# Performance work log

Hardware: AMD Instinct MI355X
Metric: run time of the kernel (lower is better)

## Reference

```python
import jax, jax.numpy as jnp
import numpy as np

DIM = 512
EXP = 2
INNER = EXP * DIM            # 1024
QKV_BLOCK = 64
NH = INNER // QKV_BLOCK      # 16 heads
DH = QKV_BLOCK               # 64 head dim
B, S = 2, 2048
KSZ = 4                      # causal conv kernel size
EPS = 5e-5                   # backend eps
NORM_EPS = 1e-6
CAP = 15.0                   # gate soft cap


def setup_inputs() -> dict:
    key = jax.random.key(0)
    ks = jax.random.split(key, 10)
    sc = lambda d: (2.0 / (5.0 * d)) ** 0.5  # small_init std
    b_if = jnp.concatenate([jnp.zeros(NH), jnp.linspace(3.0, 6.0, NH)]).astype(jnp.float32)
    return {
        "x": jax.random.normal(ks[0], (B, S, DIM), jnp.float32),
        "W_up": (jax.random.normal(ks[1], (2 * INNER, DIM), jnp.float32) * sc(DIM)),
        "W_q": (jax.random.normal(ks[2], (NH, DH, DH), jnp.float32) * sc(DH)),
        "W_k": (jax.random.normal(ks[3], (NH, DH, DH), jnp.float32) * sc(DH)),
        "W_v": (jax.random.normal(ks[4], (NH, DH, DH), jnp.float32) * sc(DH)),
        "conv_w": (jax.random.normal(ks[5], (INNER, KSZ), jnp.float32) * (1.0 / KSZ ** 0.5)),
        "conv_b": jnp.zeros((INNER,), jnp.float32),
        "W_if": (jax.random.normal(ks[6], (2 * NH, 3 * INNER), jnp.float32) * 0.02),
        "b_if": b_if,
        "norm_w": jnp.zeros((INNER,), jnp.float32),  # residual weight: gain = 1 + w
        "skip": jnp.ones((INNER,), jnp.float32),
        "W_down": (jax.random.normal(ks[7], (DIM, INNER), jnp.float32) * (2.0 / 15.0 / INNER ** 0.5)),
    }


def _headwise(x, W):
    # x: (B,S,INNER) -> per-head block-diagonal projection with W: (NH,DH,DH)
    xh = x.reshape(*x.shape[:-1], NH, DH)
    yh = jnp.einsum('bsnd,nod->bsno', xh, W)
    return yh.reshape(*x.shape[:-1], INNER)


def _causal_conv1d(x, w, b):
    # depthwise causal conv along S; x: (B,S,C), w: (C,K), b: (C,)
    xp = jnp.pad(x, ((0, 0), (KSZ - 1, 0), (0, 0)))
    y = b
    for j in range(KSZ):  # fixed tiny kernel loop
        y = y + xp[:, j:j + S, :] * w[:, j]
    return y


def _mlstm_parallel(q, k, v, i, f):
    # q,k,v: (B,NH,S,DH); i,f: (B,NH,S). Stabilized parallel mLSTM (native chunkwise math).
    logf = jax.nn.log_sigmoid(f)
    Fc = jnp.cumsum(logf, axis=-1)                              # (B,NH,S)
    logD = Fc[:, :, :, None] - Fc[:, :, None, :] + i[:, :, None, :]
    mask = jnp.tril(jnp.ones((S, S), bool))
    logD = jnp.where(mask, logD, -jnp.inf)
    m = jnp.max(logD, axis=-1)                                  # (B,NH,S), finite (diag = i[t])
    D = jnp.exp(logD - m[..., None])
    Smat = jnp.einsum('bnsd,bntd->bnst', q, k) * (DH ** -0.5)
    C = Smat * D
    n = jnp.maximum(jnp.abs(C.sum(axis=-1)), jnp.exp(-m))       # normalizer
    return jnp.einsum('bnst,bntd->bnsd', C, v) / (n + EPS)[..., None]


def reference(x, W_up, W_q, W_k, W_v, conv_w, conv_b, W_if, b_if, norm_w, skip, W_down):
    # up-projection and gate split
    x_inner = jnp.einsum('bsd,ed->bse', x, W_up)                # (B,S,2*INNER)
    x_mlstm, z = x_inner[..., :INNER], x_inner[..., INNER:]

    # causal depthwise conv + SiLU
    x_conv_act = jax.nn.silu(_causal_conv1d(x_mlstm, conv_w, conv_b))

    # headwise q,k,v
    q = _headwise(x_conv_act, W_q)
    k = _headwise(x_conv_act, W_k)
    v = _headwise(x_mlstm, W_v)

    # gate preactivations with soft cap
    if_pre = jnp.einsum('bse,ge->bsg', jnp.concatenate([q, k, v], axis=-1), W_if) + b_if
    if_pre = CAP * jnp.tanh(if_pre / CAP)
    i_pre, f_pre = if_pre[..., :NH], if_pre[..., NH:]           # (B,S,NH)
    i_g = i_pre.transpose(0, 2, 1)                              # (B,NH,S)
    f_g = f_pre.transpose(0, 2, 1)

    qh = q.reshape(B, S, NH, DH).transpose(0, 2, 1, 3)
    kh = k.reshape(B, S, NH, DH).transpose(0, 2, 1, 3)
    vh = v.reshape(B, S, NH, DH).transpose(0, 2, 1, 3)

    h = _mlstm_parallel(qh, kh, vh, i_g, f_g)                   # (B,NH,S,DH)

    # multi-head RMSNorm with residual gain (1 + w)
    rrms = jax.lax.rsqrt(jnp.mean(h * h, axis=-1, keepdims=True) + NORM_EPS)
    gain = (1.0 + norm_w).reshape(1, NH, 1, DH)
    h_norm = (h * rrms * gain).transpose(0, 2, 1, 3).reshape(B, S, INNER)

    # learnable skip, output gate, down-projection
    h_tilde = h_norm + skip * x_conv_act
    h_out = h_tilde * jax.nn.silu(z)
    return jnp.einsum('bse,de->bsd', h_out, W_down)
```

## Files before the change

### kernel.cpp

```cpp
#include <hip/hip_runtime.h>
#include <math.h>

constexpr int DIM_   = 512;
constexpr int INNER_ = 1024;
constexpr int NHEAD  = 16;
constexpr int BATCH  = 2;
constexpr int SEQ_   = 2048;
constexpr int TOK    = BATCH * SEQ_;
constexpr float EPS_ = 5e-5f;
constexpr float NEPS = 1e-6f;
constexpr float CAPV = 15.0f;

typedef __bf16 bf16_t;
typedef __attribute__((ext_vector_type(8)))  __bf16 bf16x8;
typedef __attribute__((ext_vector_type(4)))  __bf16 bf16x4;
typedef __attribute__((ext_vector_type(16))) float  f32x16;

template<int BM, int BN, int WM, int WN, int MODE>
__global__ __launch_bounds__(256) void gemm_split(const float* __restrict__ A,
    const float* __restrict__ B, float* __restrict__ C,
    int K, int lda, int ldb, int ldc)
{
    constexpr bool HAS_AL = (MODE >= 2), HAS_BL = (MODE >= 3);
    constexpr int TM = WM / 32, TN = WN / 32, NWC = BN / WN;
    __shared__ __align__(16) bf16_t sAh[BM * 32];
    __shared__ __align__(16) bf16_t sBh[BN * 32];
    __shared__ __align__(16) bf16_t sAl[HAS_AL ? BM * 32 : 8];
    __shared__ __align__(16) bf16_t sBl[HAS_BL ? BN * 32 : 8];
    const int bm = blockIdx.y * BM, bn = blockIdx.x * BN;
    const int tid = threadIdx.x, w = tid >> 6, l = tid & 63;
    const int l31 = l & 31, lh = l >> 5;
    const int wr = w / NWC, wc = w % NWC;
    f32x16 acc[TM][TN];
#pragma unroll
    for (int i = 0; i < TM; ++i)
#pragma unroll
        for (int j = 0; j < TN; ++j)
#pragma unroll
            for (int r = 0; r < 16; ++r) acc[i][j][r] = 0.f;

    for (int k0 = 0; k0 < K; k0 += 32) {
#pragma unroll
        for (int it = 0; it < BM * 4 / 256; ++it) {
            int gi = tid + it * 256; int row = gi >> 2, g = gi & 3;
            const float* src = A + (size_t)(bm + row) * lda + k0 + g * 8;
            float4 u0 = *(const float4*)src, u1 = *(const float4*)(src + 4);
            float va[8] = {u0.x, u0.y, u0.z, u0.w, u1.x, u1.y, u1.z, u1.w};
            bf16x8 h, lo2;
#pragma unroll
            for (int e = 0; e < 8; ++e) {
                bf16_t hv = (bf16_t)va[e]; h[e] = hv;
                if constexpr (HAS_AL) lo2[e] = (bf16_t)(va[e] - (float)hv);
            }
            int off = row * 32 + ((g ^ (row & 3)) << 3);
            *(bf16x8*)&sAh[off] = h;
            if constexpr (HAS_AL) *(bf16x8*)&sAl[off] = lo2;
        }
#pragma unroll
        for (int it = 0; it < BN * 4 / 256; ++it) {
            int gi = tid + it * 256; int row = gi >> 2, g = gi & 3;
            const float* src = B + (size_t)(bn + row) * ldb + k0 + g * 8;
            float4 u0 = *(const float4*)src, u1 = *(const float4*)(src + 4);
            float va[8] = {u0.x, u0.y, u0.z, u0.w, u1.x, u1.y, u1.z, u1.w};
            bf16x8 h, lo2;
#pragma unroll
            for (int e = 0; e < 8; ++e) {
                bf16_t hv = (bf16_t)va[e]; h[e] = hv;
                if constexpr (HAS_BL) lo2[e] = (bf16_t)(va[e] - (float)hv);
            }
            int off = row * 32 + ((g ^ (row & 3)) << 3);
            *(bf16x8*)&sBh[off] = h;
            if constexpr (HAS_BL) *(bf16x8*)&sBl[off] = lo2;
        }
        __syncthreads();
#pragma unroll
        for (int ks = 0; ks < 2; ++ks) {
            const int gk = 2 * ks + lh;
            bf16x8 af[TM], alf[TM], bfv[TN], blf[TN];
#pragma unroll
            for (int i = 0; i < TM; ++i) {
                int row = wr * WM + i * 32 + l31;
                int off = row * 32 + ((gk ^ (row & 3)) << 3);
                af[i] = *(const bf16x8*)&sAh[off];
                if constexpr (HAS_AL) alf[i] = *(const bf16x8*)&sAl[off];
            }
#pragma unroll
            for (int j = 0; j < TN; ++j) {
                int row = wc * WN + j * 32 + l31;
                int off = row * 32 + ((gk ^ (row & 3)) << 3);
                bfv[j] = *(const bf16x8*)&sBh[off];
                if constexpr (HAS_BL) blf[j] = *(const bf16x8*)&sBl[off];
            }
#pragma unroll
            for (int i = 0; i < TM; ++i)
#pragma unroll
                for (int j = 0; j < TN; ++j) {
                    acc[i][j] = __builtin_amdgcn_mfma_f32_32x32x16_bf16(af[i], bfv[j], acc[i][j], 0, 0, 0);
                    if constexpr (HAS_AL)
                        acc[i][j] = __builtin_amdgcn_mfma_f32_32x32x16_bf16(alf[i], bfv[j], acc[i][j], 0, 0, 0);
                    if constexpr (HAS_BL)
                        acc[i][j] = __builtin_amdgcn_mfma_f32_32x32x16_bf16(af[i], blf[j], acc[i][j], 0, 0, 0);
                }
        }
        __syncthreads();
    }
#pragma unroll
    for (int i = 0; i < TM; ++i)
#pragma unroll
        for (int j = 0; j < TN; ++j)
#pragma unroll
            for (int r = 0; r < 16; ++r) {
                int row = bm + wr * WM + i * 32 + (r & 3) + 8 * (r >> 2) + 4 * lh;
                int col = bn + wc * WN + j * 32 + l31;
                C[(size_t)row * ldc + col] = acc[i][j][r];
            }
}

__global__ __launch_bounds__(256) void conv_silu_k(const float* __restrict__ xin,
    const float* __restrict__ cw, const float* __restrict__ cb, float* __restrict__ xca)
{
    const int c = blockIdx.x * 256 + threadIdx.x;
    const int t = blockIdx.y;
    const int s = t & (SEQ_ - 1);
    const float w0 = cw[c*4+0], w1 = cw[c*4+1], w2 = cw[c*4+2], w3 = cw[c*4+3];
    const float* base = xin + (size_t)t * 2048 + c;
    float acc = cb[c];
    if (s >= 3) acc += base[-3*2048] * w0;
    if (s >= 2) acc += base[-2*2048] * w1;
    if (s >= 1) acc += base[-1*2048] * w2;
    acc += base[0] * w3;
    float sg = 1.f / (1.f + __expf(-acc));
    xca[(size_t)t * INNER_ + c] = acc * sg;
}

__global__ __launch_bounds__(256) void wif_cvt(const float* __restrict__ W_if,
    bf16_t* __restrict__ wif16)
{
    int i4 = blockIdx.x * 256 + threadIdx.x;
    float4 v = *(const float4*)(W_if + (size_t)i4 * 4);
    bf16x4 o; o[0]=(bf16_t)v.x; o[1]=(bf16_t)v.y; o[2]=(bf16_t)v.z; o[3]=(bf16_t)v.w;
    *(bf16x4*)(wif16 + (size_t)i4 * 4) = o;
}

__global__ __launch_bounds__(256) void qkv_mfma(const float* __restrict__ xca,
    const float* __restrict__ xin, const float* __restrict__ Wq,
    const float* __restrict__ Wk, const float* __restrict__ Wv,
    bf16_t* __restrict__ qb16, bf16_t* __restrict__ kb16,
    bf16_t* __restrict__ vb16, bf16_t* __restrict__ vbt16)
{
    __shared__ __align__(16) bf16_t Xs[128 * 64];
    __shared__ __align__(16) bf16_t Ws[64 * 64];
    const int mt = blockIdx.x, n = blockIdx.y, which = blockIdx.z;
    const int t0 = mt * 128, b = t0 >> 11, s0 = t0 & (SEQ_ - 1);
    const float* X = (which == 2) ? xin : xca;
    const size_t xpitch = (which == 2) ? 2048 : 1024;
    const float* W = ((which == 0) ? Wq : (which == 1) ? Wk : Wv) + n * 4096;
    const int tid = threadIdx.x, w = tid >> 6, l = tid & 63, l31 = l & 31, lh = l >> 5;
    const size_t gbn = (size_t)(b * NHEAD + n) * SEQ_;

#pragma unroll
    for (int it = 0; it < 4; ++it) {
        int gi = tid + it * 256; int row = gi >> 3, g = gi & 7;
        const float* src = X + (size_t)(t0 + row) * xpitch + n * 64 + g * 8;
        float4 u0 = *(const float4*)src, u1 = *(const float4*)(src + 4);
        float va[8] = {u0.x, u0.y, u0.z, u0.w, u1.x, u1.y, u1.z, u1.w};
        bf16x8 h;
#pragma unroll
        for (int e = 0; e < 8; ++e) h[e] = (bf16_t)va[e];
        *(bf16x8*)&Xs[row * 64 + ((g ^ (row & 7)) << 3)] = h;
    }
#pragma unroll
    for (int it = 0; it < 2; ++it) {
        int gi = tid + it * 256; int row = gi >> 3, g = gi & 7;
        const float* src = W + row * 64 + g * 8;
        float4 u0 = *(const float4*)src, u1 = *(const float4*)(src + 4);
        float va[8] = {u0.x, u0.y, u0.z, u0.w, u1.x, u1.y, u1.z, u1.w};
        bf16x8 h;
#pragma unroll
        for (int e = 0; e < 8; ++e) h[e] = (bf16_t)va[e];
        *(bf16x8*)&Ws[row * 64 + ((g ^ (row & 7)) << 3)] = h;
    }
    __syncthreads();

    if (which < 2) {
        const int wr = w >> 1, wc = w & 1;
        f32x16 acc[2];
#pragma unroll
        for (int i = 0; i < 2; ++i)
#pragma unroll
            for (int r = 0; r < 16; ++r) acc[i][r] = 0.f;
#pragma unroll
        for (int ks = 0; ks < 4; ++ks) {
            const int gk = 2 * ks + lh;
            const int wrow = wc * 32 + l31;
            bf16x8 bfrag = *(const bf16x8*)&Ws[wrow * 64 + ((gk ^ (wrow & 7)) << 3)];
#pragma unroll
            for (int i = 0; i < 2; ++i) {
                int row = wr * 64 + i * 32 + l31;
                bf16x8 afrag = *(const bf16x8*)&Xs[row * 64 + ((gk ^ (row & 7)) << 3)];
                acc[i] = __builtin_amdgcn_mfma_f32_32x32x16_bf16(afrag, bfrag, acc[i], 0, 0, 0);
            }
        }
        bf16_t* dst = which ? kb16 : qb16;
#pragma unroll
        for (int i = 0; i < 2; ++i)
#pragma unroll
            for (int r = 0; r < 16; ++r) {
                int srow = wr * 64 + i * 32 + (r & 3) + 8 * (r >> 2) + 4 * lh;
                dst[(gbn + s0 + srow) * 64 + wc * 32 + l31] = (bf16_t)acc[i][r];
            }
    } else {
        const int dh = w >> 1, th = w & 1;
        f32x16 acc[2];
#pragma unroll
        for (int j = 0; j < 2; ++j)
#pragma unroll
            for (int r = 0; r < 16; ++r) acc[j][r] = 0.f;
#pragma unroll
        for (int ks = 0; ks < 4; ++ks) {
            const int gk = 2 * ks + lh;
            const int wrow = dh * 32 + l31;
            bf16x8 afrag = *(const bf16x8*)&Ws[wrow * 64 + ((gk ^ (wrow & 7)) << 3)];
#pragma unroll
            for (int j = 0; j < 2; ++j) {
                int xrow = th * 64 + j * 32 + l31;
                bf16x8 bfrag = *(const bf16x8*)&Xs[xrow * 64 + ((gk ^ (xrow & 7)) << 3)];
                acc[j] = __builtin_amdgcn_mfma_f32_32x32x16_bf16(afrag, bfrag, acc[j], 0, 0, 0);
            }
        }
        const size_t vtb = (size_t)(b * NHEAD + n) * 64;
#pragma unroll
        for (int j = 0; j < 2; ++j)
#pragma unroll
            for (int r = 0; r < 16; ++r) {
                int drow = dh * 32 + (r & 3) + 8 * (r >> 2) + 4 * lh;
                int tcol = th * 64 + j * 32 + l31;
                vbt16[(vtb + drow) * SEQ_ + s0 + tcol] = (bf16_t)acc[j][r];
            }
        __syncthreads();
#pragma unroll
        for (int j = 0; j < 2; ++j)
#pragma unroll
            for (int r = 0; r < 16; ++r) {
                int tokrow = th * 64 + j * 32 + l31;
                int d = dh * 32 + (r & 3) + 8 * (r >> 2) + 4 * lh;
                Xs[tokrow * 64 + ((((d >> 3) ^ (tokrow & 7))) << 3) + (d & 7)] = (bf16_t)acc[j][r];
            }
        __syncthreads();
#pragma unroll
        for (int it = 0; it < 4; ++it) {
            int gi = tid + it * 256; int row = gi >> 3, g = gi & 7;
            bf16x8 v = *(const bf16x8*)&Xs[row * 64 + ((g ^ (row & 7)) << 3)];
            *(bf16x8*)&vb16[(gbn + s0 + row) * 64 + g * 8] = v;
        }
    }
}

__global__ __launch_bounds__(256) void if_mfma(const bf16_t* __restrict__ qb16,
    const bf16_t* __restrict__ kb16, const bf16_t* __restrict__ vb16,
    const bf16_t* __restrict__ wif16, float* __restrict__ ifp)
{
    __shared__ float red[4][32][33];
    const int t0g = blockIdx.x * 32;
    const int b = t0g >> 11, s0 = t0g & (SEQ_ - 1);
    const int tid = threadIdx.x, w = tid >> 6, l = tid & 63, l31 = l & 31, lh = l >> 5;
    const size_t base0 = (size_t)b * NHEAD * SEQ_ * 64 + (size_t)(s0 + l31) * 64;
    const bf16_t* wbase = wif16 + (size_t)l31 * 3072 + 8 * lh;
    f32x16 acc;
#pragma unroll
    for (int r = 0; r < 16; ++r) acc[r] = 0.f;
#pragma unroll 4
    for (int it = 0; it < 48; ++it) {
        const int kg = w * 768 + it * 16;
        const int which = kg >> 10, rem = kg & 1023;
        const int head = rem >> 6, dd = (rem & 63) + 8 * lh;
        const bf16_t* src = (which == 0) ? qb16 : (which == 1) ? kb16 : vb16;
        bf16x8 af = *(const bf16x8*)(src + base0 + (size_t)head * SEQ_ * 64 + dd);
        bf16x8 bf = *(const bf16x8*)(wbase + kg);
        acc = __builtin_amdgcn_mfma_f32_32x32x16_bf16(af, bf, acc, 0, 0, 0);
    }
#pragma unroll
    for (int r = 0; r < 16; ++r) {
        int row = (r & 3) + 8 * (r >> 2) + 4 * lh;
        red[w][row][l31] = acc[r];
    }
    __syncthreads();
#pragma unroll
    for (int it = 0; it < 4; ++it) {
        int idx = tid + it * 256;
        int row = idx >> 5, col = idx & 31;
        float s = red[0][row][col] + red[1][row][col] + red[2][row][col] + red[3][row][col];
        ifp[(size_t)(t0g + row) * 32 + col] = s;
    }
}

__global__ __launch_bounds__(256) void gate_scan(const float* __restrict__ ifp,
    const float* __restrict__ b_if, float* __restrict__ aval,
    float* __restrict__ cmaxv, float* __restrict__ emv)
{
    __shared__ float tots[256];
    const int bn = blockIdx.x;
    const int b = bn >> 4, n = bn & 15;
    const int tid = threadIdx.x;
    const float bi = b_if[n], bf = b_if[16 + n];
    const int s0 = tid * 8;
    float iv[8], lf[8];
#pragma unroll
    for (int j = 0; j < 8; ++j) {
        size_t row = ((size_t)b * SEQ_ + s0 + j) * 32;
        float ip = ifp[row + n] + bi;        ip = CAPV * tanhf(ip * (1.f / CAPV));
        float fp = ifp[row + 16 + n] + bf;   fp = CAPV * tanhf(fp * (1.f / CAPV));
        float ls = fminf(fp, 0.f) - log1pf(expf(-fabsf(fp)));
        iv[j] = ip; lf[j] = ls;
    }
#pragma unroll
    for (int j = 1; j < 8; ++j) lf[j] += lf[j-1];
    tots[tid] = lf[7];
    __syncthreads();
    for (int off = 1; off < 256; off <<= 1) {
        float o = (tid >= off) ? tots[tid - off] : 0.f;
        __syncthreads();
        tots[tid] += o;
        __syncthreads();
    }
    const float exs = (tid > 0) ? tots[tid - 1] : 0.f;
    float Fc[8], a[8], am[8];
#pragma unroll
    for (int j = 0; j < 8; ++j) { Fc[j] = exs + lf[j]; a[j] = iv[j] - Fc[j]; }
    am[0] = a[0];
#pragma unroll
    for (int j = 1; j < 8; ++j) am[j] = fmaxf(am[j-1], a[j]);
    __syncthreads();
    tots[tid] = am[7];
    __syncthreads();
    for (int off = 1; off < 256; off <<= 1) {
        float o = (tid >= off) ? tots[tid - off] : -INFINITY;
        __syncthreads();
        tots[tid] = fmaxf(tots[tid], o);
        __syncthreads();
    }
    const float exm = (tid > 0) ? tots[tid - 1] : -INFINITY;
    const size_t base = (size_t)bn * SEQ_ + s0;
#pragma unroll
    for (int j = 0; j < 8; ++j) {
        float cm = fmaxf(exm, am[j]);
        aval[base + j]  = a[j];
        cmaxv[base + j] = cm;
        emv[base + j]   = expf(-(Fc[j] + cm));
    }
}

__global__ __launch_bounds__(256, 3) void mlstm_k2(
    const bf16_t* __restrict__ qb16, const bf16_t* __restrict__ kb16,
    const bf16_t* __restrict__ vbt16,
    const float* __restrict__ aval, const float* __restrict__ cmaxv,
    const float* __restrict__ emv, const float* __restrict__ xca,
    const float* __restrict__ xin, const float* __restrict__ norm_w,
    const float* __restrict__ skipv, float* __restrict__ houtp)
{
    __shared__ bf16_t ks[64*64];
    __shared__ bf16_t vts[64*64];
    __shared__ bf16_t Ps[64*64];
    __shared__ float a_sh[64], cm_sh[64], em_sh[64], nw_sh[64], sk_sh[64];
    __shared__ float red_lds[2][2][2][16];

    const int st = (int)gridDim.x - 1 - (int)blockIdx.x;
    const int n = blockIdx.y, b = blockIdx.z;
    const int tid = threadIdx.x;
    const int w = tid >> 6, l = tid & 63;
    const int rh = w >> 1, th = w & 1;
    const int l31 = l & 31, lh = l >> 5;
    const size_t gb = (size_t)(b * NHEAD + n) * SEQ_;

    if (tid < 64) {
        cm_sh[tid] = cmaxv[gb + st*64 + tid];
        em_sh[tid] = emv[gb + st*64 + tid];
        nw_sh[tid] = 1.f + norm_w[n*64 + tid];
        sk_sh[tid] = skipv[n*64 + tid];
    }
    bf16x8 qf[4];
    {
        const bf16_t* qp = qb16 + (gb + (size_t)st*64 + 32*rh + l31) * 64 + 8*lh;
#pragma unroll
        for (int kc = 0; kc < 4; ++kc) qf[kc] = *(const bf16x8*)(qp + 16*kc);
    }
    f32x16 hac, csum;
#pragma unroll
    for (int i = 0; i < 16; ++i) { hac[i] = 0.f; csum[i] = 0.f; }
    __syncthreads();

    for (int tt = 0; tt <= st; ++tt) {
        {
            const bf16_t* kgp = kb16 + (gb + (size_t)tt*64) * 64;
            const bf16_t* vgp = vbt16 + (size_t)(b * NHEAD + n) * 64 * SEQ_ + (size_t)tt*64;
#pragma unroll
            for (int it = 0; it < 2; ++it) {
                int id = tid + it * 256;
                int r = id >> 3, c = (id & 7) << 3;
                int sw = c ^ ((r & 7) << 3);
                bf16x8 kv = *(const bf16x8*)(kgp + r*64 + c);
                *(bf16x8*)(&ks[r*64 + sw]) = kv;
                bf16x8 vv = *(const bf16x8*)(vgp + (size_t)r * SEQ_ + c);
                *(bf16x8*)(&vts[r*64 + sw]) = vv;
            }
            if (tid < 64) a_sh[tid] = aval[gb + tt*64 + tid];
        }
        __syncthreads();
        f32x16 acc;
#pragma unroll
        for (int i = 0; i < 16; ++i) acc[i] = 0.f;
        {
            const int r = l31 + 32*th;
            const int swb = (r & 7) << 3;
#pragma unroll
            for (int kc = 0; kc < 4; ++kc) {
                bf16x8 bk = *(const bf16x8*)(&ks[r*64 + ((8*lh + 16*kc) ^ swb)]);
                acc = __builtin_amdgcn_mfma_f32_32x32x16_bf16(qf[kc], bk, acc, 0, 0, 0);
            }
        }
        {
            const int tcol = l31 + 32*th;
            const float aw = a_sh[tcol];
            const bool diag = (tt == st);
#pragma unroll
            for (int reg = 0; reg < 16; ++reg) {
                const int srow = (reg & 3) + 8*(reg >> 2) + 4*lh + 32*rh;
                float wgt = 0.125f * __expf(aw - cm_sh[srow]);
                if (diag && tcol > srow) wgt = 0.f;
                float p = acc[reg] * wgt;
                csum[reg] += p;
                Ps[srow*64 + (tcol ^ ((srow & 7) << 3))] = (bf16_t)p;
            }
        }
        __syncthreads();
        {
            const int pr = l31 + 32*rh, vr = l31 + 32*th;
            const int swp = (pr & 7) << 3, swv = (vr & 7) << 3;
#pragma unroll
            for (int kc = 0; kc < 4; ++kc) {
                const int d0 = 8*lh + 16*kc;
                bf16x8 ap = *(const bf16x8*)(&Ps[pr*64 + (d0 ^ swp)]);
                bf16x8 bv = *(const bf16x8*)(&vts[vr*64 + (d0 ^ swv)]);
                hac = __builtin_amdgcn_mfma_f32_32x32x16_bf16(ap, bv, hac, 0, 0, 0);
            }
        }
        __syncthreads();
    }

#pragma unroll
    for (int reg = 0; reg < 16; ++reg) {
        float c = csum[reg];
        c += __shfl_xor(c, 1); c += __shfl_xor(c, 2); c += __shfl_xor(c, 4);
        c += __shfl_xor(c, 8); c += __shfl_xor(c, 16);
        csum[reg] = c;
    }
    if (l31 == 0) {
#pragma unroll
        for (int reg = 0; reg < 16; ++reg) red_lds[rh][th][lh][reg] = csum[reg];
    }
    __syncthreads();
    float sqv[16];
#pragma unroll
    for (int reg = 0; reg < 16; ++reg) {
        const int srow = (reg & 3) + 8*(reg >> 2) + 4*lh + 32*rh;
        float ct = red_lds[rh][0][lh][reg] + red_lds[rh][1][lh][reg];
        float iv = 1.f / (fmaxf(fabsf(ct), em_sh[srow]) + EPS_);
        hac[reg] *= iv;
        sqv[reg] = hac[reg] * hac[reg];
    }
    __syncthreads();
#pragma unroll
    for (int reg = 0; reg < 16; ++reg) {
        float sq = sqv[reg];
        sq += __shfl_xor(sq, 1); sq += __shfl_xor(sq, 2); sq += __shfl_xor(sq, 4);
        sq += __shfl_xor(sq, 8); sq += __shfl_xor(sq, 16);
        sqv[reg] = sq;
    }
    if (l31 == 0) {
#pragma unroll
        for (int reg = 0; reg < 16; ++reg) red_lds[rh][th][lh][reg] = sqv[reg];
    }
    __syncthreads();
    {
        const int dcol = l31 + 32*th;
        const float gn = nw_sh[dcol], sk = sk_sh[dcol];
        const int col = n*64 + dcol;
#pragma unroll
        for (int reg = 0; reg < 16; ++reg) {
            const int srow = (reg & 3) + 8*(reg >> 2) + 4*lh + 32*rh;
            float sq = red_lds[rh][0][lh][reg] + red_lds[rh][1][lh][reg];
            float rr = rsqrtf(sq * (1.f/64.f) + NEPS);
            const size_t tok = (size_t)b * SEQ_ + (size_t)st*64 + srow;
            float ht = hac[reg] * rr * gn + sk * xca[tok * INNER_ + col];
            float zz = xin[tok * 2048 + 1024 + col];
            float sil = zz / (1.f + __expf(-zz));
            houtp[tok * 2048 + col] = ht * sil;
        }
    }
}

extern "C" void kernel_launch(void* const* d_in, const int* in_sizes, int n_in,
                              void* d_out, int out_size, void* d_ws, size_t ws_size,
                              hipStream_t stream)
{
    const float* x      = (const float*)d_in[0];
    const float* W_up   = (const float*)d_in[1];
    const float* W_q    = (const float*)d_in[2];
    const float* W_k    = (const float*)d_in[3];
    const float* W_v    = (const float*)d_in[4];
    const float* conv_w = (const float*)d_in[5];
    const float* conv_b = (const float*)d_in[6];
    const float* W_if   = (const float*)d_in[7];
    const float* b_if   = (const float*)d_in[8];
    const float* norm_w = (const float*)d_in[9];
    const float* skip   = (const float*)d_in[10];
    const float* W_down = (const float*)d_in[11];
    float* out = (float*)d_out;

    float* xin   = (float*)d_ws;
    float* xca   = xin  + (size_t)TOK * 2048;
    float* ifp   = xca  + (size_t)TOK * INNER_;
    float* aval  = ifp  + (size_t)TOK * 32;
    float* cmaxv = aval + (size_t)BATCH * NHEAD * SEQ_;
    float* emv   = cmaxv+ (size_t)BATCH * NHEAD * SEQ_;
    bf16_t* qb16 = (bf16_t*)(emv + (size_t)BATCH * NHEAD * SEQ_);
    bf16_t* kb16 = qb16 + (size_t)TOK * INNER_;
    bf16_t* vb16 = kb16 + (size_t)TOK * INNER_;
    bf16_t* vbt16= vb16 + (size_t)TOK * INNER_;
    bf16_t* wif16= vbt16+ (size_t)TOK * INNER_;

    gemm_split<128,128,64,64,3><<<dim3(2048/128, TOK/128), 256, 0, stream>>>(
        x, W_up, xin, DIM_, DIM_, DIM_, 2048);
    conv_silu_k<<<dim3(INNER_/256, TOK), 256, 0, stream>>>(xin, conv_w, conv_b, xca);
    wif_cvt<<<dim3(96), 256, 0, stream>>>(W_if, wif16);
    qkv_mfma<<<dim3(TOK/128, NHEAD, 3), 256, 0, stream>>>(xca, xin, W_q, W_k, W_v,
        qb16, kb16, vb16, vbt16);
    if_mfma<<<dim3(TOK/32), 256, 0, stream>>>(qb16, kb16, vb16, wif16, ifp);
    gate_scan<<<dim3(BATCH*NHEAD), 256, 0, stream>>>(ifp, b_if, aval, cmaxv, emv);
    mlstm_k2<<<dim3(SEQ_/64, NHEAD, BATCH), 256, 0, stream>>>(qb16, kb16, vbt16,
        aval, cmaxv, emv, xca, xin, norm_w, skip, xin );
    gemm_split<128,64,32,64,3><<<dim3(DIM_/64, TOK/128), 256, 0, stream>>>(
        xin, W_down, out, INNER_, 2048, INNER_, DIM_);
}
```

Before: 331.7 us.

## Factor decay weights into pre-scaled K and keep P in registers

```diff
diff --git a/kernel.cpp b/kernel.cpp
--- a/kernel.cpp
+++ b/kernel.cpp
@@ -15,6 +15,7 @@
 typedef __attribute__((ext_vector_type(8)))  __bf16 bf16x8;
 typedef __attribute__((ext_vector_type(4)))  __bf16 bf16x4;
 typedef __attribute__((ext_vector_type(16))) float  f32x16;
+typedef __attribute__((ext_vector_type(4)))  unsigned int u32x4;
 
 template<int BM, int BN, int WM, int WN, int MODE>
 __global__ __launch_bounds__(256) void gemm_split(const float* __restrict__ A,
@@ -295,10 +296,11 @@
 }
 
 __global__ __launch_bounds__(256) void gate_scan(const float* __restrict__ ifp,
-    const float* __restrict__ b_if, float* __restrict__ aval,
+    const float* __restrict__ b_if, float* __restrict__ colfac,
     float* __restrict__ cmaxv, float* __restrict__ emv)
 {
     __shared__ float tots[256];
+    __shared__ float cmE[32];
     const int bn = blockIdx.x;
     const int b = bn >> 4, n = bn & 15;
     const int tid = threadIdx.x;
@@ -340,162 +342,175 @@
         __syncthreads();
     }
     const float exm = (tid > 0) ? tots[tid - 1] : -INFINITY;
+    if ((tid & 7) == 7) cmE[tid >> 3] = fmaxf(exm, am[7]);
+    __syncthreads();
+    const float ce = cmE[tid >> 3];
     const size_t base = (size_t)bn * SEQ_ + s0;
 #pragma unroll
     for (int j = 0; j < 8; ++j) {
         float cm = fmaxf(exm, am[j]);
-        aval[base + j]  = a[j];
-        cmaxv[base + j] = cm;
-        emv[base + j]   = expf(-(Fc[j] + cm));
-    }
-}
-
-__global__ __launch_bounds__(256, 3) void mlstm_k2(
-    const bf16_t* __restrict__ qb16, const bf16_t* __restrict__ kb16,
+        colfac[base + j] = __expf(a[j] - ce);
+        cmaxv[base + j]  = cm;
+        emv[base + j]    = expf(-(Fc[j] + cm));
+    }
+}
+
+__global__ __launch_bounds__(256) void kscale(bf16_t* __restrict__ kb16,
+    const float* __restrict__ colfac)
+{
+    const int i = blockIdx.x * 256 + threadIdx.x;
+    const int row = i >> 3, c = (i & 7) << 3;
+    const float cf = 0.125f * colfac[row];
+    bf16x8 v = *(const bf16x8*)(kb16 + (size_t)row * 64 + c);
+#pragma unroll
+    for (int e = 0; e < 8; ++e) v[e] = (bf16_t)((float)v[e] * cf);
+    *(bf16x8*)(kb16 + (size_t)row * 64 + c) = v;
+}
+
+__device__ inline unsigned pack2(float a, float b) {
+    union { bf16_t h; unsigned short u; } ua, ub;
+    ua.h = (bf16_t)a; ub.h = (bf16_t)b;
+    return (unsigned)ua.u | ((unsigned)ub.u << 16);
+}
+
+__global__ __launch_bounds__(256, 3) void mlstm_k3(
+    const bf16_t* __restrict__ qb16, const bf16_t* __restrict__ khat,
     const bf16_t* __restrict__ vbt16,
-    const float* __restrict__ aval, const float* __restrict__ cmaxv,
-    const float* __restrict__ emv, const float* __restrict__ xca,
-    const float* __restrict__ xin, const float* __restrict__ norm_w,
-    const float* __restrict__ skipv, float* __restrict__ houtp)
-{
-    __shared__ bf16_t ks[64*64];
-    __shared__ bf16_t vts[64*64];
-    __shared__ bf16_t Ps[64*64];
-    __shared__ float a_sh[64], cm_sh[64], em_sh[64], nw_sh[64], sk_sh[64];
+    const float* __restrict__ cmaxv, const float* __restrict__ emv,
+    const float* __restrict__ xca, const float* __restrict__ xin,
+    const float* __restrict__ norm_w, const float* __restrict__ skipv,
+    float* __restrict__ houtp)
+{
+    __shared__ __align__(16) bf16_t ks[2][64*64];
+    __shared__ __align__(16) bf16_t vts[2][64*64];
+    __shared__ float cmB_sh[32];
+    __shared__ float inv_lds[64];
     __shared__ float red_lds[2][2][2][16];
 
     const int st = (int)gridDim.x - 1 - (int)blockIdx.x;
     const int n = blockIdx.y, b = blockIdx.z;
-    const int tid = threadIdx.x;
-    const int w = tid >> 6, l = tid & 63;
-    const int rh = w >> 1, th = w & 1;
+    const int tid = threadIdx.x, w = tid >> 6, l = tid & 63;
     const int l31 = l & 31, lh = l >> 5;
+    const int sh = w >> 1, dh = w & 1;
     const size_t gb = (size_t)(b * NHEAD + n) * SEQ_;
-
-    if (tid < 64) {
-        cm_sh[tid] = cmaxv[gb + st*64 + tid];
-        em_sh[tid] = emv[gb + st*64 + tid];
-        nw_sh[tid] = 1.f + norm_w[n*64 + tid];
-        sk_sh[tid] = skipv[n*64 + tid];
-    }
+    const int s_lane = 32 * sh + l31;
+    const int d_lane = 32 * dh + l31;
+
+    const float cmq = cmaxv[gb + (size_t)st * 64 + s_lane];
+    const float emq = emv[gb + (size_t)st * 64 + s_lane];
+    const int col = n * 64 + d_lane;
+    const float gn = 1.f + norm_w[col];
+    const float sk = skipv[col];
+    if (tid < 32) cmB_sh[tid] = cmaxv[gb + (size_t)tid * 64 + 63];
+
     bf16x8 qf[4];
     {
-        const bf16_t* qp = qb16 + (gb + (size_t)st*64 + 32*rh + l31) * 64 + 8*lh;
-#pragma unroll
-        for (int kc = 0; kc < 4; ++kc) qf[kc] = *(const bf16x8*)(qp + 16*kc);
-    }
-    f32x16 hac, csum;
-#pragma unroll
-    for (int i = 0; i < 16; ++i) { hac[i] = 0.f; csum[i] = 0.f; }
-    __syncthreads();
-
+        const bf16_t* qp = qb16 + (gb + (size_t)st * 64 + s_lane) * 64 + 8 * lh;
+#pragma unroll
+        for (int kc = 0; kc < 4; ++kc) qf[kc] = *(const bf16x8*)(qp + 16 * kc);
+    }
+    f32x16 hac;
+#pragma unroll
+    for (int i = 0; i < 16; ++i) hac[i] = 0.f;
+    float csum = 0.f;
+
+    const bf16_t* kbase = khat + gb * 64;
+    const bf16_t* vbase = vbt16 + (size_t)(b * NHEAD + n) * 64 * SEQ_;
+
+#define STAGE(buf, ttv) { \
+    const bf16_t* kgp = kbase + (size_t)(ttv) * 64 * 64; \
+    const bf16_t* vgp = vbase + (size_t)(ttv) * 64; \
+    _Pragma("unroll") \
+    for (int it_ = 0; it_ < 2; ++it_) { \
+        int id_ = tid + it_ * 256; \
+        int r_ = id_ >> 3, c_ = (id_ & 7) << 3; \
+        int sw_ = c_ ^ ((r_ & 7) << 3); \
+        *(bf16x8*)&ks[buf][r_ * 64 + sw_] = *(const bf16x8*)(kgp + r_ * 64 + c_); \
+        *(bf16x8*)&vts[buf][r_ * 64 + sw_] = *(const bf16x8*)(vgp + (size_t)r_ * SEQ_ + c_); \
+    } }
+
+    STAGE(0, 0)
+    int cur = 0;
     for (int tt = 0; tt <= st; ++tt) {
-        {
-            const bf16_t* kgp = kb16 + (gb + (size_t)tt*64) * 64;
-            const bf16_t* vgp = vbt16 + (size_t)(b * NHEAD + n) * 64 * SEQ_ + (size_t)tt*64;
-#pragma unroll
-            for (int it = 0; it < 2; ++it) {
-                int id = tid + it * 256;
-                int r = id >> 3, c = (id & 7) << 3;
-                int sw = c ^ ((r & 7) << 3);
-                bf16x8 kv = *(const bf16x8*)(kgp + r*64 + c);
-                *(bf16x8*)(&ks[r*64 + sw]) = kv;
-                bf16x8 vv = *(const bf16x8*)(vgp + (size_t)r * SEQ_ + c);
-                *(bf16x8*)(&vts[r*64 + sw]) = vv;
-            }
-            if (tid < 64) a_sh[tid] = aval[gb + tt*64 + tid];
-        }
-        __syncthreads();
-        f32x16 acc;
-#pragma unroll
-        for (int i = 0; i < 16; ++i) acc[i] = 0.f;
-        {
-            const int r = l31 + 32*th;
-            const int swb = (r & 7) << 3;
+        __syncthreads();
+        if (tt < st) STAGE(cur ^ 1, tt + 1)
+        const float rf = __expf(cmB_sh[tt] - cmq);
+        const bool diag = (tt == st);
+#pragma unroll
+        for (int tq = 0; tq < 2; ++tq) {
+            if (diag && sh == 0 && tq == 1) continue;
+            f32x16 p;
+#pragma unroll
+            for (int i = 0; i < 16; ++i) p[i] = 0.f;
+            const int krow = 32 * tq + l31;
+            const int swk = (krow & 7) << 3;
 #pragma unroll
             for (int kc = 0; kc < 4; ++kc) {
-                bf16x8 bk = *(const bf16x8*)(&ks[r*64 + ((8*lh + 16*kc) ^ swb)]);
-                acc = __builtin_amdgcn_mfma_f32_32x32x16_bf16(qf[kc], bk, acc, 0, 0, 0);
-            }
-        }
-        {
-            const int tcol = l31 + 32*th;
-            const float aw = a_sh[tcol];
-            const bool diag = (tt == st);
+                bf16x8 kf = *(const bf16x8*)&ks[cur][krow * 64 + ((8 * lh + 16 * kc) ^ swk)];
+                p = __builtin_amdgcn_mfma_f32_32x32x16_bf16(kf, qf[kc], p, 0, 0, 0);
+            }
 #pragma unroll
             for (int reg = 0; reg < 16; ++reg) {
-                const int srow = (reg & 3) + 8*(reg >> 2) + 4*lh + 32*rh;
-                float wgt = 0.125f * __expf(aw - cm_sh[srow]);
-                if (diag && tcol > srow) wgt = 0.f;
-                float p = acc[reg] * wgt;
-                csum[reg] += p;
-                Ps[srow*64 + (tcol ^ ((srow & 7) << 3))] = (bf16_t)p;
-            }
-        }
-        __syncthreads();
-        {
-            const int pr = l31 + 32*rh, vr = l31 + 32*th;
-            const int swp = (pr & 7) << 3, swv = (vr & 7) << 3;
-#pragma unroll
-            for (int kc = 0; kc < 4; ++kc) {
-                const int d0 = 8*lh + 16*kc;
-                bf16x8 ap = *(const bf16x8*)(&Ps[pr*64 + (d0 ^ swp)]);
-                bf16x8 bv = *(const bf16x8*)(&vts[vr*64 + (d0 ^ swv)]);
-                hac = __builtin_amdgcn_mfma_f32_32x32x16_bf16(ap, bv, hac, 0, 0, 0);
-            }
-        }
-        __syncthreads();
-    }
-
+                const int t_loc = (reg & 3) + 8 * (reg >> 2) + 4 * lh + 32 * tq;
+                float pw = p[reg] * rf;
+                if (diag && t_loc > s_lane) pw = 0.f;
+                csum += pw;
+                p[reg] = pw;
+            }
+            unsigned W0 = pack2(p[0],  p[1]),  W1 = pack2(p[2],  p[3]);
+            unsigned W2 = pack2(p[4],  p[5]),  W3 = pack2(p[6],  p[7]);
+            unsigned W4 = pack2(p[8],  p[9]),  W5 = pack2(p[10], p[11]);
+            unsigned W6 = pack2(p[12], p[13]), W7 = pack2(p[14], p[15]);
+            unsigned r1 = __shfl_xor(lh ? W0 : W2, 32, 64);
+            unsigned r2 = __shfl_xor(lh ? W1 : W3, 32, 64);
+            unsigned r3 = __shfl_xor(lh ? W4 : W6, 32, 64);
+            unsigned r4 = __shfl_xor(lh ? W5 : W7, 32, 64);
+            u32x4 pa0 = lh ? (u32x4){r1, r2, W2, W3} : (u32x4){W0, W1, r1, r2};
+            u32x4 pa1 = lh ? (u32x4){r3, r4, W6, W7} : (u32x4){W4, W5, r3, r4};
+            const int swv = (d_lane & 7) << 3;
+#pragma unroll
+            for (int kcl = 0; kcl < 2; ++kcl) {
+                const int kcg = 2 * tq + kcl;
+                bf16x8 vf = *(const bf16x8*)&vts[cur][d_lane * 64 + ((8 * lh + 16 * kcg) ^ swv)];
+                bf16x8 paf = __builtin_bit_cast(bf16x8, kcl ? pa1 : pa0);
+                hac = __builtin_amdgcn_mfma_f32_32x32x16_bf16(paf, vf, hac, 0, 0, 0);
+            }
+        }
+        cur ^= 1;
+    }
+#undef STAGE
+
+    csum += __shfl_xor(csum, 32, 64);
+    const float ivv = 1.f / (fmaxf(fabsf(csum), emq) + EPS_);
+    if (dh == 0 && lh == 0) inv_lds[s_lane] = ivv;
+    __syncthreads();
+    float sq[16];
 #pragma unroll
     for (int reg = 0; reg < 16; ++reg) {
-        float c = csum[reg];
-        c += __shfl_xor(c, 1); c += __shfl_xor(c, 2); c += __shfl_xor(c, 4);
-        c += __shfl_xor(c, 8); c += __shfl_xor(c, 16);
-        csum[reg] = c;
+        const int s_loc = (reg & 3) + 8 * (reg >> 2) + 4 * lh;
+        float h = hac[reg] * inv_lds[32 * sh + s_loc];
+        hac[reg] = h;
+        float s2 = h * h;
+        s2 += __shfl_xor(s2, 1);  s2 += __shfl_xor(s2, 2);
+        s2 += __shfl_xor(s2, 4);  s2 += __shfl_xor(s2, 8);
+        s2 += __shfl_xor(s2, 16);
+        sq[reg] = s2;
     }
     if (l31 == 0) {
 #pragma unroll
-        for (int reg = 0; reg < 16; ++reg) red_lds[rh][th][lh][reg] = csum[reg];
-    }
-    __syncthreads();
-    float sqv[16];
+        for (int reg = 0; reg < 16; ++reg) red_lds[sh][dh][lh][reg] = sq[reg];
+    }
+    __syncthreads();
 #pragma unroll
     for (int reg = 0; reg < 16; ++reg) {
-        const int srow = (reg & 3) + 8*(reg >> 2) + 4*lh + 32*rh;
-        float ct = red_lds[rh][0][lh][reg] + red_lds[rh][1][lh][reg];
-        float iv = 1.f / (fmaxf(fabsf(ct), em_sh[srow]) + EPS_);
-        hac[reg] *= iv;
-        sqv[reg] = hac[reg] * hac[reg];
-    }
-    __syncthreads();
-#pragma unroll
-    for (int reg = 0; reg < 16; ++reg) {
-        float sq = sqv[reg];
-        sq += __shfl_xor(sq, 1); sq += __shfl_xor(sq, 2); sq += __shfl_xor(sq, 4);
-        sq += __shfl_xor(sq, 8); sq += __shfl_xor(sq, 16);
-        sqv[reg] = sq;
-    }
-    if (l31 == 0) {
-#pragma unroll
-        for (int reg = 0; reg < 16; ++reg) red_lds[rh][th][lh][reg] = sqv[reg];
-    }
-    __syncthreads();
-    {
-        const int dcol = l31 + 32*th;
-        const float gn = nw_sh[dcol], sk = sk_sh[dcol];
-        const int col = n*64 + dcol;
-#pragma unroll
-        for (int reg = 0; reg < 16; ++reg) {
-            const int srow = (reg & 3) + 8*(reg >> 2) + 4*lh + 32*rh;
-            float sq = red_lds[rh][0][lh][reg] + red_lds[rh][1][lh][reg];
-            float rr = rsqrtf(sq * (1.f/64.f) + NEPS);
-            const size_t tok = (size_t)b * SEQ_ + (size_t)st*64 + srow;
-            float ht = hac[reg] * rr * gn + sk * xca[tok * INNER_ + col];
-            float zz = xin[tok * 2048 + 1024 + col];
-            float sil = zz / (1.f + __expf(-zz));
-            houtp[tok * 2048 + col] = ht * sil;
-        }
+        const int s_loc = (reg & 3) + 8 * (reg >> 2) + 4 * lh;
+        const float ssq = red_lds[sh][0][lh][reg] + red_lds[sh][1][lh][reg];
+        const float rr = rsqrtf(ssq * (1.f / 64.f) + NEPS);
+        const size_t tok = (size_t)b * SEQ_ + (size_t)st * 64 + 32 * sh + s_loc;
+        float ht = hac[reg] * rr * gn + sk * xca[tok * INNER_ + col];
+        float zz = xin[tok * 2048 + 1024 + col];
+        float sil = zz / (1.f + __expf(-zz));
+        houtp[tok * 2048 + col] = ht * sil;
     }
 }
 
@@ -517,17 +532,17 @@
     const float* W_down = (const float*)d_in[11];
     float* out = (float*)d_out;
 
-    float* xin   = (float*)d_ws;
-    float* xca   = xin  + (size_t)TOK * 2048;
-    float* ifp   = xca  + (size_t)TOK * INNER_;
-    float* aval  = ifp  + (size_t)TOK * 32;
-    float* cmaxv = aval + (size_t)BATCH * NHEAD * SEQ_;
-    float* emv   = cmaxv+ (size_t)BATCH * NHEAD * SEQ_;
-    bf16_t* qb16 = (bf16_t*)(emv + (size_t)BATCH * NHEAD * SEQ_);
-    bf16_t* kb16 = qb16 + (size_t)TOK * INNER_;
-    bf16_t* vb16 = kb16 + (size_t)TOK * INNER_;
-    bf16_t* vbt16= vb16 + (size_t)TOK * INNER_;
-    bf16_t* wif16= vbt16+ (size_t)TOK * INNER_;
+    float* xin    = (float*)d_ws;
+    float* xca    = xin  + (size_t)TOK * 2048;
+    float* ifp    = xca  + (size_t)TOK * INNER_;
+    float* colfac = ifp  + (size_t)TOK * 32;
+    float* cmaxv  = colfac + (size_t)BATCH * NHEAD * SEQ_;
+    float* emv    = cmaxv  + (size_t)BATCH * NHEAD * SEQ_;
+    bf16_t* qb16  = (bf16_t*)(emv + (size_t)BATCH * NHEAD * SEQ_);
+    bf16_t* kb16  = qb16 + (size_t)TOK * INNER_;
+    bf16_t* vb16  = kb16 + (size_t)TOK * INNER_;
+    bf16_t* vbt16 = vb16 + (size_t)TOK * INNER_;
+    bf16_t* wif16 = vbt16+ (size_t)TOK * INNER_;
 
     gemm_split<128,128,64,64,3><<<dim3(2048/128, TOK/128), 256, 0, stream>>>(
         x, W_up, xin, DIM_, DIM_, DIM_, 2048);
@@ -536,9 +551,10 @@
     qkv_mfma<<<dim3(TOK/128, NHEAD, 3), 256, 0, stream>>>(xca, xin, W_q, W_k, W_v,
         qb16, kb16, vb16, vbt16);
     if_mfma<<<dim3(TOK/32), 256, 0, stream>>>(qb16, kb16, vb16, wif16, ifp);
-    gate_scan<<<dim3(BATCH*NHEAD), 256, 0, stream>>>(ifp, b_if, aval, cmaxv, emv);
-    mlstm_k2<<<dim3(SEQ_/64, NHEAD, BATCH), 256, 0, stream>>>(qb16, kb16, vbt16,
-        aval, cmaxv, emv, xca, xin, norm_w, skip, xin );
+    gate_scan<<<dim3(BATCH*NHEAD), 256, 0, stream>>>(ifp, b_if, colfac, cmaxv, emv);
+    kscale<<<dim3(TOK*INNER_/8/256), 256, 0, stream>>>(kb16, colfac);
+    mlstm_k3<<<dim3(SEQ_/64, NHEAD, BATCH), 256, 0, stream>>>(qb16, kb16, vbt16,
+        cmaxv, emv, xca, xin, norm_w, skip, xin );
     gemm_split<128,64,32,64,3><<<dim3(DIM_/64, TOK/128), 256, 0, stream>>>(
         xin, W_down, out, INNER_, 2048, INNER_, DIM_);
 }
```

Result: faster. 303.6 us (-8.5%).
